# Kernel optimization log

Hardware: AMD Instinct MI355X
Metric: run time of the kernel (lower is better)

Reference implementation:

```python
import jax, jax.numpy as jnp
import numpy as np

B = 16384
D = 64            # embed_dim
N_LAYER = 2
USER_NUM, ITEM_NUM, ENTITY_NUM = 500000, 200000, 200000
H1, H2 = 128, 64  # hidden_layers
OUT_REC = 1


def setup_inputs() -> dict:
    key = jax.random.key(0)
    ks = jax.random.split(key, 24)
    f = jax.random.normal
    return {
        "user_id": jax.random.randint(ks[0], (B,), 0, USER_NUM),
        "item_id": jax.random.randint(ks[1], (B,), 0, ITEM_NUM),
        "rec_target": jax.random.uniform(ks[2], (B,), dtype=jnp.float32),
        # embedding tables
        "user_emb": f(ks[3], (USER_NUM, D), dtype=jnp.float32) * 0.01,
        "item_emb": f(ks[4], (ITEM_NUM, D), dtype=jnp.float32) * 0.01,
        "entity_emb": f(ks[5], (ENTITY_NUM, D), dtype=jnp.float32) * 0.01,
        # cross&compress parameters (torch.rand -> uniform [0,1))
        "w_vv": jax.random.uniform(ks[6], (D, 1), dtype=jnp.float32),
        "w_ev": jax.random.uniform(ks[7], (D, 1), dtype=jnp.float32),
        "w_ve": jax.random.uniform(ks[8], (D, 1), dtype=jnp.float32),
        "w_ee": jax.random.uniform(ks[9], (D, 1), dtype=jnp.float32),
        "b_v": jax.random.uniform(ks[10], (1,), dtype=jnp.float32),
        "b_e": jax.random.uniform(ks[11], (1,), dtype=jnp.float32),
        # user low MLP (embed_dim -> embed_dim)
        "Wul": f(ks[12], (D, D), dtype=jnp.float32) * (1.0 / np.sqrt(D)),
        "bul": jnp.zeros((D,), dtype=jnp.float32),
        # rec tower: 2D -> H1 -> H2 -> OUT_REC
        "W1": f(ks[13], (2 * D, H1), dtype=jnp.float32) * (1.0 / np.sqrt(2 * D)),
        "b1": jnp.zeros((H1,), dtype=jnp.float32),
        "W2": f(ks[14], (H1, H2), dtype=jnp.float32) * (1.0 / np.sqrt(H1)),
        "b2": jnp.zeros((H2,), dtype=jnp.float32),
        "W3": f(ks[15], (H2, OUT_REC), dtype=jnp.float32) * (1.0 / np.sqrt(H2)),
        "b3": jnp.zeros((OUT_REC,), dtype=jnp.float32),
    }


def _cross_compress(item, head, w_vv, w_ev, w_ve, w_ee, b_v, b_e):
    # c = item[:, :, None] * head[:, None, :]; c @ w == item * (head @ w)
    # c_t = head[:, :, None] * item[:, None, :]; c_t @ w == head * (item @ w)
    item_c = item * (head @ w_vv) + head * (item @ w_ev) + b_v
    head_c = item * (head @ w_ve) + head * (item @ w_ee) + b_e
    return item_c, head_c


def reference(user_id, item_id, rec_target, user_emb, item_emb, entity_emb,
              w_vv, w_ev, w_ve, w_ee, b_v, b_e, Wul, bul,
              W1, b1, W2, b2, W3, b3):
    # 'rec' training path (dropout disabled / eval mode)
    user = user_emb[user_id]      # [B, D]
    item = item_emb[item_id]      # [B, D]
    head = entity_emb[item_id]    # [B, D]
    for _ in range(N_LAYER):
        user = jax.nn.relu(user @ Wul + bul)
        item, head = _cross_compress(item, head, w_vv, w_ev, w_ve, w_ee, b_v, b_e)
    high = jnp.concatenate([user, item], axis=1)          # [B, 2D]
    h = jax.nn.relu(high @ W1 + b1)
    h = jax.nn.relu(h @ W2 + b2)
    rec_out = jax.nn.relu(h @ W3 + b3)                    # [B, 1]
    return rec_out.squeeze(-1), rec_target
```

## Files before the change

### kernel.cpp

```cpp
#include <hip/hip_runtime.h>


constexpr int BTOT = 16384;
constexpr int SPB  = 16;
constexpr int PAD  = 20;

__global__ __launch_bounds__(256, 4) void multikr_fused(
    const int* __restrict__ user_id, const int* __restrict__ item_id,
    const float* __restrict__ rec_target,
    const float* __restrict__ user_emb, const float* __restrict__ item_emb,
    const float* __restrict__ entity_emb,
    const float* __restrict__ w_vv, const float* __restrict__ w_ev,
    const float* __restrict__ w_ve, const float* __restrict__ w_ee,
    const float* __restrict__ b_v, const float* __restrict__ b_e,
    const float* __restrict__ Wul, const float* __restrict__ bul,
    const float* __restrict__ W1, const float* __restrict__ b1,
    const float* __restrict__ W2, const float* __restrict__ b2,
    const float* __restrict__ W3, const float* __restrict__ b3,
    float* __restrict__ out)
{
    __shared__ __align__(16) float sm[256 * PAD];
    __shared__ __align__(16) float sWul[64 * 64];
    __shared__ __align__(16) float wcT[4][64];
    __shared__ __align__(16) float scal[4][SPB];

    const int t    = threadIdx.x;
    const int lane = t & 63;
    const int wv   = t >> 6;
    const int aoff = wv << 2;
    const int s0   = blockIdx.x * SPB;

    float* U  = sm;
    float* IT = sm + 64 * PAD;
    float* HD = sm + 128 * PAD;
    float* SP = sm + 192 * PAD;

    {
        const int s = t & 15, part = t >> 4;
        const int uid = user_id[s0 + s], iid = item_id[s0 + s];
        const float4 u4 = *((const float4*)(user_emb   + (size_t)uid * 64) + part);
        const float4 i4 = *((const float4*)(item_emb   + (size_t)iid * 64) + part);
        const float4 e4 = *((const float4*)(entity_emb + (size_t)iid * 64) + part);
        const int db = part << 2;
        U [(db+0)*PAD+s]=u4.x; U [(db+1)*PAD+s]=u4.y; U [(db+2)*PAD+s]=u4.z; U [(db+3)*PAD+s]=u4.w;
        IT[(db+0)*PAD+s]=i4.x; IT[(db+1)*PAD+s]=i4.y; IT[(db+2)*PAD+s]=i4.z; IT[(db+3)*PAD+s]=i4.w;
        HD[(db+0)*PAD+s]=e4.x; HD[(db+1)*PAD+s]=e4.y; HD[(db+2)*PAD+s]=e4.z; HD[(db+3)*PAD+s]=e4.w;
        const float4* wg = (const float4*)Wul;
        float4*       ws = (float4*)sWul;
#pragma unroll
        for (int i = 0; i < 4; ++i) ws[i * 256 + t] = wg[i * 256 + t];
        if (t < 64) { wcT[0][t]=w_vv[t]; wcT[1][t]=w_ev[t]; wcT[2][t]=w_ve[t]; wcT[3][t]=w_ee[t]; }
    }
    __syncthreads();
    const float bv = b_v[0], be = b_e[0];

#pragma unroll
    for (int layer = 0; layer < 2; ++layer) {
        const float* ub = (layer == 0) ? U : SP;
        float*       vb = (layer == 0) ? SP : U;
        {
            float ua[4];
            const float bb = bul[lane];
#pragma unroll
            for (int i = 0; i < 4; ++i) ua[i] = bb;
#pragma unroll 8
            for (int d = 0; d < 64; ++d) {
                const float w = sWul[d * 64 + lane];
                const float4 av = *(const float4*)(ub + d * PAD + aoff);
                ua[0]=fmaf(av.x,w,ua[0]); ua[1]=fmaf(av.y,w,ua[1]);
                ua[2]=fmaf(av.z,w,ua[2]); ua[3]=fmaf(av.w,w,ua[3]);
            }
            *(float4*)(vb + lane * PAD + aoff) =
                make_float4(fmaxf(ua[0],0.f),fmaxf(ua[1],0.f),fmaxf(ua[2],0.f),fmaxf(ua[3],0.f));
        }
        if (lane < 16) {
            const float* src = (wv & 1) ? IT : HD;
            float a = 0.f;
#pragma unroll
            for (int dq = 0; dq < 16; ++dq) {
                const float4 w = *(const float4*)&wcT[wv][dq << 2];
                a = fmaf(src[(4*dq+0)*PAD + lane], w.x, a);
                a = fmaf(src[(4*dq+1)*PAD + lane], w.y, a);
                a = fmaf(src[(4*dq+2)*PAD + lane], w.z, a);
                a = fmaf(src[(4*dq+3)*PAD + lane], w.w, a);
            }
            scal[wv][lane] = a;
        }
        __syncthreads();
        {
            float* ip = IT + lane * PAD + aoff;
            float* hp = HD + lane * PAD + aoff;
            const float4 iv = *(const float4*)ip;
            const float4 hv = *(const float4*)hp;
            const float4 sa = *(const float4*)&scal[0][aoff];
            const float4 sb = *(const float4*)&scal[1][aoff];
            *(float4*)ip = make_float4(
                fmaf(iv.x, sa.x, fmaf(hv.x, sb.x, bv)),
                fmaf(iv.y, sa.y, fmaf(hv.y, sb.y, bv)),
                fmaf(iv.z, sa.z, fmaf(hv.z, sb.z, bv)),
                fmaf(iv.w, sa.w, fmaf(hv.w, sb.w, bv)));
            if (layer == 0) {
                const float4 sc = *(const float4*)&scal[2][aoff];
                const float4 sd = *(const float4*)&scal[3][aoff];
                *(float4*)hp = make_float4(
                    fmaf(iv.x, sc.x, fmaf(hv.x, sd.x, be)),
                    fmaf(iv.y, sc.y, fmaf(hv.y, sd.y, be)),
                    fmaf(iv.z, sc.z, fmaf(hv.z, sd.z, be)),
                    fmaf(iv.w, sc.w, fmaf(hv.w, sd.w, be)));
            }
        }
        __syncthreads();
    }

    {
        float acc0[4], acc1[4];
        const float bb0 = b1[lane], bb1 = b1[lane + 64];
#pragma unroll
        for (int i = 0; i < 4; ++i) { acc0[i] = bb0; acc1[i] = bb1; }
        float wA[16], wB[16];
        auto ldg = [&](float* buf, int dbase) {
#pragma unroll
            for (int k = 0; k < 8; ++k) {
                buf[2*k]   = W1[(dbase + k) * 128 + lane];
                buf[2*k+1] = W1[(dbase + k) * 128 + lane + 64];
            }
        };
        auto cmp = [&](const float* buf, int dbase) {
#pragma unroll
            for (int k = 0; k < 8; ++k) {
                const float4 av = *(const float4*)(sm + (dbase + k) * PAD + aoff);
                const float w0 = buf[2*k], w1 = buf[2*k+1];
                acc0[0]=fmaf(av.x,w0,acc0[0]); acc0[1]=fmaf(av.y,w0,acc0[1]);
                acc0[2]=fmaf(av.z,w0,acc0[2]); acc0[3]=fmaf(av.w,w0,acc0[3]);
                acc1[0]=fmaf(av.x,w1,acc1[0]); acc1[1]=fmaf(av.y,w1,acc1[1]);
                acc1[2]=fmaf(av.z,w1,acc1[2]); acc1[3]=fmaf(av.w,w1,acc1[3]);
            }
        };
        ldg(wA, 0);
#pragma unroll
        for (int g = 0; g < 8; ++g) {
            ldg(wB, 16*g + 8);
            cmp(wA, 16*g);
            if (g < 7) ldg(wA, 16*g + 16);
            cmp(wB, 16*g + 8);
        }
        *(float4*)(sm + (128 + lane) * PAD + aoff) =
            make_float4(fmaxf(acc0[0],0.f),fmaxf(acc0[1],0.f),fmaxf(acc0[2],0.f),fmaxf(acc0[3],0.f));
        *(float4*)(sm + (192 + lane) * PAD + aoff) =
            make_float4(fmaxf(acc1[0],0.f),fmaxf(acc1[1],0.f),fmaxf(acc1[2],0.f),fmaxf(acc1[3],0.f));
    }
    __syncthreads();

    {
        float acc[4];
        const float bb = b2[lane];
#pragma unroll
        for (int i = 0; i < 4; ++i) acc[i] = bb;
        float wA[8], wB[8];
        auto ldg = [&](float* buf, int dbase) {
#pragma unroll
            for (int k = 0; k < 8; ++k) buf[k] = W2[(dbase + k) * 64 + lane];
        };
        auto cmp = [&](const float* buf, int dbase) {
#pragma unroll
            for (int k = 0; k < 8; ++k) {
                const float4 av = *(const float4*)(sm + (128 + dbase + k) * PAD + aoff);
                const float w = buf[k];
                acc[0]=fmaf(av.x,w,acc[0]); acc[1]=fmaf(av.y,w,acc[1]);
                acc[2]=fmaf(av.z,w,acc[2]); acc[3]=fmaf(av.w,w,acc[3]);
            }
        };
        ldg(wA, 0);
#pragma unroll
        for (int g = 0; g < 8; ++g) {
            ldg(wB, 16*g + 8);
            cmp(wA, 16*g);
            if (g < 7) ldg(wA, 16*g + 16);
            cmp(wB, 16*g + 8);
        }
        *(float4*)(sm + lane * PAD + aoff) =
            make_float4(fmaxf(acc[0],0.f),fmaxf(acc[1],0.f),fmaxf(acc[2],0.f),fmaxf(acc[3],0.f));
    }
    __syncthreads();

    if (t < 64) {
        const int s = t & 15, dh = t >> 4;
        float acc = 0.f;
#pragma unroll
        for (int k = 0; k < 16; ++k) {
            const int d = 16 * dh + k;
            acc = fmaf(sm[d * PAD + s], W3[d], acc);
        }
        acc += __shfl_xor(acc, 16);
        acc += __shfl_xor(acc, 32);
        if (dh == 0) out[s0 + s] = fmaxf(acc + b3[0], 0.f);
    } else if (t < 80) {
        const int s = t - 64;
        out[BTOT + s0 + s] = rec_target[s0 + s];
    }
}

extern "C" void kernel_launch(void* const* d_in, const int* in_sizes, int n_in,
                              void* d_out, int out_size, void* d_ws, size_t ws_size,
                              hipStream_t stream) {
    (void)in_sizes; (void)n_in; (void)d_ws; (void)ws_size; (void)out_size;
    multikr_fused<<<BTOT / SPB, 256, 0, stream>>>(
        (const int*)d_in[0],  (const int*)d_in[1],  (const float*)d_in[2],
        (const float*)d_in[3], (const float*)d_in[4], (const float*)d_in[5],
        (const float*)d_in[6], (const float*)d_in[7], (const float*)d_in[8],
        (const float*)d_in[9], (const float*)d_in[10], (const float*)d_in[11],
        (const float*)d_in[12], (const float*)d_in[13], (const float*)d_in[14],
        (const float*)d_in[15], (const float*)d_in[16], (const float*)d_in[17],
        (const float*)d_in[18], (const float*)d_in[19],
        (float*)d_out);
}
```

Baseline: 258.9 us.

## Double samples per block and use register tiles in MLP layers

Raises samples per block from 16 to 32 (with a matching pad and a lower occupancy hint) and remaps the thread work so each thread computes larger register tiles: 2x4 in the user layer, 4x4 in the W1 layer and 4x2 in the W2 layer, using float4 weight loads. Cross-compress weights and W3 are kept in registers and the dot products are split over two half-waves with a shuffle reduction. The goal is to halve the per-sample global weight traffic and the number of LDS reads per FMA. In exchange the block count halves, shared memory per block roughly doubles, and register pressure rises.

Result: no change. 259.8 us (+0.3%).

```diff
diff --git a/kernel.cpp b/kernel.cpp
--- a/kernel.cpp
+++ b/kernel.cpp
@@ -2,10 +2,10 @@
 
 
 constexpr int BTOT = 16384;
-constexpr int SPB  = 16;
-constexpr int PAD  = 20;
-
-__global__ __launch_bounds__(256, 4) void multikr_fused(
+constexpr int SPB  = 32;
+constexpr int PAD  = 36;
+
+__global__ __launch_bounds__(256, 2) void multikr_fused(
     const int* __restrict__ user_id, const int* __restrict__ item_id,
     const float* __restrict__ rec_target,
     const float* __restrict__ user_emb, const float* __restrict__ item_emb,
@@ -21,13 +21,11 @@
 {
     __shared__ __align__(16) float sm[256 * PAD];
     __shared__ __align__(16) float sWul[64 * 64];
-    __shared__ __align__(16) float wcT[4][64];
     __shared__ __align__(16) float scal[4][SPB];
 
     const int t    = threadIdx.x;
     const int lane = t & 63;
     const int wv   = t >> 6;
-    const int aoff = wv << 2;
     const int s0   = blockIdx.x * SPB;
 
     float* U  = sm;
@@ -35,168 +33,210 @@
     float* HD = sm + 128 * PAD;
     float* SP = sm + 192 * PAD;
 
-    {
-        const int s = t & 15, part = t >> 4;
+    const int dh   = lane >> 5;
+    const int sdot = lane & 31;
+
+    float wcr[32];
+    {
+        const float* wsrc = (wv == 0) ? w_vv : (wv == 1) ? w_ev : (wv == 2) ? w_ve : w_ee;
+#pragma unroll
+        for (int q = 0; q < 8; ++q) {
+            const float4 w4 = *(const float4*)(wsrc + 32 * dh + 4 * q);
+            wcr[4*q] = w4.x; wcr[4*q+1] = w4.y; wcr[4*q+2] = w4.z; wcr[4*q+3] = w4.w;
+        }
+    }
+
+    {
+        const int s = t & 31, p = t >> 5;
         const int uid = user_id[s0 + s], iid = item_id[s0 + s];
-        const float4 u4 = *((const float4*)(user_emb   + (size_t)uid * 64) + part);
-        const float4 i4 = *((const float4*)(item_emb   + (size_t)iid * 64) + part);
-        const float4 e4 = *((const float4*)(entity_emb + (size_t)iid * 64) + part);
-        const int db = part << 2;
-        U [(db+0)*PAD+s]=u4.x; U [(db+1)*PAD+s]=u4.y; U [(db+2)*PAD+s]=u4.z; U [(db+3)*PAD+s]=u4.w;
-        IT[(db+0)*PAD+s]=i4.x; IT[(db+1)*PAD+s]=i4.y; IT[(db+2)*PAD+s]=i4.z; IT[(db+3)*PAD+s]=i4.w;
-        HD[(db+0)*PAD+s]=e4.x; HD[(db+1)*PAD+s]=e4.y; HD[(db+2)*PAD+s]=e4.z; HD[(db+3)*PAD+s]=e4.w;
+        const float4* ur = (const float4*)(user_emb   + (size_t)uid * 64 + 8 * p);
+        const float4* ir = (const float4*)(item_emb   + (size_t)iid * 64 + 8 * p);
+        const float4* er = (const float4*)(entity_emb + (size_t)iid * 64 + 8 * p);
+        const float4 u0 = ur[0], u1 = ur[1];
+        const float4 i0 = ir[0], i1 = ir[1];
+        const float4 e0 = er[0], e1 = er[1];
+        const int db = 8 * p;
+        U [(db+0)*PAD+s]=u0.x; U [(db+1)*PAD+s]=u0.y; U [(db+2)*PAD+s]=u0.z; U [(db+3)*PAD+s]=u0.w;
+        U [(db+4)*PAD+s]=u1.x; U [(db+5)*PAD+s]=u1.y; U [(db+6)*PAD+s]=u1.z; U [(db+7)*PAD+s]=u1.w;
+        IT[(db+0)*PAD+s]=i0.x; IT[(db+1)*PAD+s]=i0.y; IT[(db+2)*PAD+s]=i0.z; IT[(db+3)*PAD+s]=i0.w;
+        IT[(db+4)*PAD+s]=i1.x; IT[(db+5)*PAD+s]=i1.y; IT[(db+6)*PAD+s]=i1.z; IT[(db+7)*PAD+s]=i1.w;
+        HD[(db+0)*PAD+s]=e0.x; HD[(db+1)*PAD+s]=e0.y; HD[(db+2)*PAD+s]=e0.z; HD[(db+3)*PAD+s]=e0.w;
+        HD[(db+4)*PAD+s]=e1.x; HD[(db+5)*PAD+s]=e1.y; HD[(db+6)*PAD+s]=e1.z; HD[(db+7)*PAD+s]=e1.w;
         const float4* wg = (const float4*)Wul;
         float4*       ws = (float4*)sWul;
 #pragma unroll
         for (int i = 0; i < 4; ++i) ws[i * 256 + t] = wg[i * 256 + t];
-        if (t < 64) { wcT[0][t]=w_vv[t]; wcT[1][t]=w_ev[t]; wcT[2][t]=w_ve[t]; wcT[3][t]=w_ee[t]; }
     }
     __syncthreads();
     const float bv = b_v[0], be = b_e[0];
 
-#pragma unroll
-    for (int layer = 0; layer < 2; ++layer) {
-        const float* ub = (layer == 0) ? U : SP;
-        float*       vb = (layer == 0) ? SP : U;
-        {
-            float ua[4];
-            const float bb = bul[lane];
-#pragma unroll
-            for (int i = 0; i < 4; ++i) ua[i] = bb;
-#pragma unroll 8
-            for (int d = 0; d < 64; ++d) {
-                const float w = sWul[d * 64 + lane];
-                const float4 av = *(const float4*)(ub + d * PAD + aoff);
-                ua[0]=fmaf(av.x,w,ua[0]); ua[1]=fmaf(av.y,w,ua[1]);
-                ua[2]=fmaf(av.z,w,ua[2]); ua[3]=fmaf(av.w,w,ua[3]);
-            }
-            *(float4*)(vb + lane * PAD + aoff) =
-                make_float4(fmaxf(ua[0],0.f),fmaxf(ua[1],0.f),fmaxf(ua[2],0.f),fmaxf(ua[3],0.f));
-        }
-        if (lane < 16) {
-            const float* src = (wv & 1) ? IT : HD;
-            float a = 0.f;
-#pragma unroll
-            for (int dq = 0; dq < 16; ++dq) {
-                const float4 w = *(const float4*)&wcT[wv][dq << 2];
-                a = fmaf(src[(4*dq+0)*PAD + lane], w.x, a);
-                a = fmaf(src[(4*dq+1)*PAD + lane], w.y, a);
-                a = fmaf(src[(4*dq+2)*PAD + lane], w.z, a);
-                a = fmaf(src[(4*dq+3)*PAD + lane], w.w, a);
-            }
-            scal[wv][lane] = a;
-        }
-        __syncthreads();
-        {
-            float* ip = IT + lane * PAD + aoff;
-            float* hp = HD + lane * PAD + aoff;
-            const float4 iv = *(const float4*)ip;
-            const float4 hv = *(const float4*)hp;
-            const float4 sa = *(const float4*)&scal[0][aoff];
-            const float4 sb = *(const float4*)&scal[1][aoff];
-            *(float4*)ip = make_float4(
-                fmaf(iv.x, sa.x, fmaf(hv.x, sb.x, bv)),
-                fmaf(iv.y, sa.y, fmaf(hv.y, sb.y, bv)),
-                fmaf(iv.z, sa.z, fmaf(hv.z, sb.z, bv)),
-                fmaf(iv.w, sa.w, fmaf(hv.w, sb.w, bv)));
-            if (layer == 0) {
-                const float4 sc = *(const float4*)&scal[2][aoff];
-                const float4 sd = *(const float4*)&scal[3][aoff];
-                *(float4*)hp = make_float4(
-                    fmaf(iv.x, sc.x, fmaf(hv.x, sd.x, be)),
-                    fmaf(iv.y, sc.y, fmaf(hv.y, sd.y, be)),
-                    fmaf(iv.z, sc.z, fmaf(hv.z, sd.z, be)),
-                    fmaf(iv.w, sc.w, fmaf(hv.w, sd.w, be)));
-            }
-        }
-        __syncthreads();
-    }
-
-    {
-        float acc0[4], acc1[4];
-        const float bb0 = b1[lane], bb1 = b1[lane + 64];
-#pragma unroll
-        for (int i = 0; i < 4; ++i) { acc0[i] = bb0; acc1[i] = bb1; }
-        float wA[16], wB[16];
-        auto ldg = [&](float* buf, int dbase) {
+    {
+        const int cg = lane & 31;
+        const int m0 = 8 * wv + 4 * (lane >> 5);
+#pragma unroll
+        for (int layer = 0; layer < 2; ++layer) {
+            const float* ub = (layer == 0) ? U : SP;
+            float*       vb = (layer == 0) ? SP : U;
+            {
+                const float2 bb = *(const float2*)(bul + 2 * cg);
+                float a0[4] = {bb.x, bb.x, bb.x, bb.x};
+                float a1[4] = {bb.y, bb.y, bb.y, bb.y};
+#pragma unroll
+                for (int d = 0; d < 64; ++d) {
+                    const float4 av = *(const float4*)(ub + d * PAD + m0);
+                    const float2 w  = *(const float2*)(sWul + d * 64 + 2 * cg);
+                    a0[0]=fmaf(av.x,w.x,a0[0]); a0[1]=fmaf(av.y,w.x,a0[1]);
+                    a0[2]=fmaf(av.z,w.x,a0[2]); a0[3]=fmaf(av.w,w.x,a0[3]);
+                    a1[0]=fmaf(av.x,w.y,a1[0]); a1[1]=fmaf(av.y,w.y,a1[1]);
+                    a1[2]=fmaf(av.z,w.y,a1[2]); a1[3]=fmaf(av.w,w.y,a1[3]);
+                }
+                *(float4*)(vb + (2*cg    ) * PAD + m0) =
+                    make_float4(fmaxf(a0[0],0.f),fmaxf(a0[1],0.f),fmaxf(a0[2],0.f),fmaxf(a0[3],0.f));
+                *(float4*)(vb + (2*cg + 1) * PAD + m0) =
+                    make_float4(fmaxf(a1[0],0.f),fmaxf(a1[1],0.f),fmaxf(a1[2],0.f),fmaxf(a1[3],0.f));
+            }
+            {
+                const float* src = (wv & 1) ? IT : HD;
+                float a = 0.f;
+#pragma unroll
+                for (int k = 0; k < 32; ++k)
+                    a = fmaf(src[(32 * dh + k) * PAD + sdot], wcr[k], a);
+                a += __shfl_xor(a, 32);
+                if (dh == 0) scal[wv][sdot] = a;
+            }
+            __syncthreads();
+            {
+                float* ip = IT + lane * PAD + 8 * wv;
+                float* hp = HD + lane * PAD + 8 * wv;
+                const float4 iv0 = *(const float4*)(ip),     iv1 = *(const float4*)(ip + 4);
+                const float4 hv0 = *(const float4*)(hp),     hv1 = *(const float4*)(hp + 4);
+                const float4 sa0 = *(const float4*)&scal[0][8*wv], sa1 = *(const float4*)&scal[0][8*wv+4];
+                const float4 sb0 = *(const float4*)&scal[1][8*wv], sb1 = *(const float4*)&scal[1][8*wv+4];
+                *(float4*)(ip) = make_float4(
+                    fmaf(iv0.x, sa0.x, fmaf(hv0.x, sb0.x, bv)),
+                    fmaf(iv0.y, sa0.y, fmaf(hv0.y, sb0.y, bv)),
+                    fmaf(iv0.z, sa0.z, fmaf(hv0.z, sb0.z, bv)),
+                    fmaf(iv0.w, sa0.w, fmaf(hv0.w, sb0.w, bv)));
+                *(float4*)(ip + 4) = make_float4(
+                    fmaf(iv1.x, sa1.x, fmaf(hv1.x, sb1.x, bv)),
+                    fmaf(iv1.y, sa1.y, fmaf(hv1.y, sb1.y, bv)),
+                    fmaf(iv1.z, sa1.z, fmaf(hv1.z, sb1.z, bv)),
+                    fmaf(iv1.w, sa1.w, fmaf(hv1.w, sb1.w, bv)));
+                if (layer == 0) {
+                    const float4 sc0 = *(const float4*)&scal[2][8*wv], sc1 = *(const float4*)&scal[2][8*wv+4];
+                    const float4 sd0 = *(const float4*)&scal[3][8*wv], sd1 = *(const float4*)&scal[3][8*wv+4];
+                    *(float4*)(hp) = make_float4(
+                        fmaf(iv0.x, sc0.x, fmaf(hv0.x, sd0.x, be)),
+                        fmaf(iv0.y, sc0.y, fmaf(hv0.y, sd0.y, be)),
+                        fmaf(iv0.z, sc0.z, fmaf(hv0.z, sd0.z, be)),
+                        fmaf(iv0.w, sc0.w, fmaf(hv0.w, sd0.w, be)));
+                    *(float4*)(hp + 4) = make_float4(
+                        fmaf(iv1.x, sc1.x, fmaf(hv1.x, sd1.x, be)),
+                        fmaf(iv1.y, sc1.y, fmaf(hv1.y, sd1.y, be)),
+                        fmaf(iv1.z, sc1.z, fmaf(hv1.z, sd1.z, be)),
+                        fmaf(iv1.w, sc1.w, fmaf(hv1.w, sd1.w, be)));
+                }
+            }
+            __syncthreads();
+        }
+    }
+
+    {
+        const int c0  = 4 * (lane & 31);
+        const int m0h = 8 * wv + 4 * (lane >> 5);
+        float acc[4][4];
+        const float4 bb = *(const float4*)(b1 + c0);
+#pragma unroll
+        for (int i = 0; i < 4; ++i) { acc[0][i]=bb.x; acc[1][i]=bb.y; acc[2][i]=bb.z; acc[3][i]=bb.w; }
+        float4 wA[8], wB[8];
+        auto ldg = [&](float4* buf, int db) {
+#pragma unroll
+            for (int k = 0; k < 8; ++k) buf[k] = *(const float4*)(W1 + (db + k) * 128 + c0);
+        };
+        auto cmp = [&](const float4* buf, int db) {
 #pragma unroll
             for (int k = 0; k < 8; ++k) {
-                buf[2*k]   = W1[(dbase + k) * 128 + lane];
-                buf[2*k+1] = W1[(dbase + k) * 128 + lane + 64];
-            }
-        };
-        auto cmp = [&](const float* buf, int dbase) {
+                const float4 av = *(const float4*)(sm + (db + k) * PAD + m0h);
+                const float4 w  = buf[k];
+                acc[0][0]=fmaf(av.x,w.x,acc[0][0]); acc[0][1]=fmaf(av.y,w.x,acc[0][1]);
+                acc[0][2]=fmaf(av.z,w.x,acc[0][2]); acc[0][3]=fmaf(av.w,w.x,acc[0][3]);
+                acc[1][0]=fmaf(av.x,w.y,acc[1][0]); acc[1][1]=fmaf(av.y,w.y,acc[1][1]);
+                acc[1][2]=fmaf(av.z,w.y,acc[1][2]); acc[1][3]=fmaf(av.w,w.y,acc[1][3]);
+                acc[2][0]=fmaf(av.x,w.z,acc[2][0]); acc[2][1]=fmaf(av.y,w.z,acc[2][1]);
+                acc[2][2]=fmaf(av.z,w.z,acc[2][2]); acc[2][3]=fmaf(av.w,w.z,acc[2][3]);
+                acc[3][0]=fmaf(av.x,w.w,acc[3][0]); acc[3][1]=fmaf(av.y,w.w,acc[3][1]);
+                acc[3][2]=fmaf(av.z,w.w,acc[3][2]); acc[3][3]=fmaf(av.w,w.w,acc[3][3]);
+            }
+        };
+        ldg(wA, 0);
+#pragma unroll
+        for (int g = 0; g < 8; ++g) {
+            ldg(wB, 16 * g + 8);
+            cmp(wA, 16 * g);
+            if (g < 7) ldg(wA, 16 * g + 16);
+            cmp(wB, 16 * g + 8);
+        }
+#pragma unroll
+        for (int c = 0; c < 4; ++c)
+            *(float4*)(sm + (128 + c0 + c) * PAD + m0h) =
+                make_float4(fmaxf(acc[c][0],0.f),fmaxf(acc[c][1],0.f),
+                            fmaxf(acc[c][2],0.f),fmaxf(acc[c][3],0.f));
+    }
+    __syncthreads();
+
+    {
+        const int c0 = 4 * (lane & 15);
+        const int m2 = 8 * wv + 2 * (lane >> 4);
+        float acc[4][2];
+        const float4 bb = *(const float4*)(b2 + c0);
+        acc[0][0]=acc[0][1]=bb.x; acc[1][0]=acc[1][1]=bb.y;
+        acc[2][0]=acc[2][1]=bb.z; acc[3][0]=acc[3][1]=bb.w;
+        float4 wA[8], wB[8];
+        auto ldg = [&](float4* buf, int db) {
+#pragma unroll
+            for (int k = 0; k < 8; ++k) buf[k] = *(const float4*)(W2 + (db + k) * 64 + c0);
+        };
+        auto cmp = [&](const float4* buf, int db) {
 #pragma unroll
             for (int k = 0; k < 8; ++k) {
-                const float4 av = *(const float4*)(sm + (dbase + k) * PAD + aoff);
-                const float w0 = buf[2*k], w1 = buf[2*k+1];
-                acc0[0]=fmaf(av.x,w0,acc0[0]); acc0[1]=fmaf(av.y,w0,acc0[1]);
-                acc0[2]=fmaf(av.z,w0,acc0[2]); acc0[3]=fmaf(av.w,w0,acc0[3]);
-                acc1[0]=fmaf(av.x,w1,acc1[0]); acc1[1]=fmaf(av.y,w1,acc1[1]);
-                acc1[2]=fmaf(av.z,w1,acc1[2]); acc1[3]=fmaf(av.w,w1,acc1[3]);
+                const float2 av = *(const float2*)(sm + (128 + db + k) * PAD + m2);
+                const float4 w  = buf[k];
+                acc[0][0]=fmaf(av.x,w.x,acc[0][0]); acc[0][1]=fmaf(av.y,w.x,acc[0][1]);
+                acc[1][0]=fmaf(av.x,w.y,acc[1][0]); acc[1][1]=fmaf(av.y,w.y,acc[1][1]);
+                acc[2][0]=fmaf(av.x,w.z,acc[2][0]); acc[2][1]=fmaf(av.y,w.z,acc[2][1]);
+                acc[3][0]=fmaf(av.x,w.w,acc[3][0]); acc[3][1]=fmaf(av.y,w.w,acc[3][1]);
             }
         };
         ldg(wA, 0);
 #pragma unroll
         for (int g = 0; g < 8; ++g) {
-            ldg(wB, 16*g + 8);
-            cmp(wA, 16*g);
-            if (g < 7) ldg(wA, 16*g + 16);
-            cmp(wB, 16*g + 8);
-        }
-        *(float4*)(sm + (128 + lane) * PAD + aoff) =
-            make_float4(fmaxf(acc0[0],0.f),fmaxf(acc0[1],0.f),fmaxf(acc0[2],0.f),fmaxf(acc0[3],0.f));
-        *(float4*)(sm + (192 + lane) * PAD + aoff) =
-            make_float4(fmaxf(acc1[0],0.f),fmaxf(acc1[1],0.f),fmaxf(acc1[2],0.f),fmaxf(acc1[3],0.f));
+            ldg(wB, 16 * g + 8);
+            cmp(wA, 16 * g);
+            if (g < 7) ldg(wA, 16 * g + 16);
+            cmp(wB, 16 * g + 8);
+        }
+#pragma unroll
+        for (int c = 0; c < 4; ++c)
+            *(float2*)(sm + (c0 + c) * PAD + m2) =
+                make_float2(fmaxf(acc[c][0],0.f), fmaxf(acc[c][1],0.f));
     }
     __syncthreads();
 
-    {
-        float acc[4];
-        const float bb = b2[lane];
-#pragma unroll
-        for (int i = 0; i < 4; ++i) acc[i] = bb;
-        float wA[8], wB[8];
-        auto ldg = [&](float* buf, int dbase) {
-#pragma unroll
-            for (int k = 0; k < 8; ++k) buf[k] = W2[(dbase + k) * 64 + lane];
-        };
-        auto cmp = [&](const float* buf, int dbase) {
-#pragma unroll
-            for (int k = 0; k < 8; ++k) {
-                const float4 av = *(const float4*)(sm + (128 + dbase + k) * PAD + aoff);
-                const float w = buf[k];
-                acc[0]=fmaf(av.x,w,acc[0]); acc[1]=fmaf(av.y,w,acc[1]);
-                acc[2]=fmaf(av.z,w,acc[2]); acc[3]=fmaf(av.w,w,acc[3]);
-            }
-        };
-        ldg(wA, 0);
-#pragma unroll
-        for (int g = 0; g < 8; ++g) {
-            ldg(wB, 16*g + 8);
-            cmp(wA, 16*g);
-            if (g < 7) ldg(wA, 16*g + 16);
-            cmp(wB, 16*g + 8);
-        }
-        *(float4*)(sm + lane * PAD + aoff) =
-            make_float4(fmaxf(acc[0],0.f),fmaxf(acc[1],0.f),fmaxf(acc[2],0.f),fmaxf(acc[3],0.f));
-    }
-    __syncthreads();
-
-    if (t < 64) {
-        const int s = t & 15, dh = t >> 4;
-        float acc = 0.f;
-#pragma unroll
-        for (int k = 0; k < 16; ++k) {
-            const int d = 16 * dh + k;
-            acc = fmaf(sm[d * PAD + s], W3[d], acc);
-        }
-        acc += __shfl_xor(acc, 16);
-        acc += __shfl_xor(acc, 32);
-        if (dh == 0) out[s0 + s] = fmaxf(acc + b3[0], 0.f);
-    } else if (t < 80) {
-        const int s = t - 64;
-        out[BTOT + s0 + s] = rec_target[s0 + s];
+    if (wv == 0) {
+        float w3r[32];
+#pragma unroll
+        for (int q = 0; q < 8; ++q) {
+            const float4 w4 = *(const float4*)(W3 + 32 * dh + 4 * q);
+            w3r[4*q] = w4.x; w3r[4*q+1] = w4.y; w3r[4*q+2] = w4.z; w3r[4*q+3] = w4.w;
+        }
+        float a = 0.f;
+#pragma unroll
+        for (int k = 0; k < 32; ++k)
+            a = fmaf(sm[(32 * dh + k) * PAD + sdot], w3r[k], a);
+        a += __shfl_xor(a, 32);
+        if (dh == 0) out[s0 + sdot] = fmaxf(a + b3[0], 0.f);
+    } else if (wv == 1) {
+        if (lane < 32) out[BTOT + s0 + lane] = rec_target[s0 + lane];
     }
 }
 
```

## Drop shared Wul staging and remap MLP thread tiles to read weights from global

Applied to the files above, without the earlier changes.

Removes the shared-memory copy of Wul and has each thread read Wul, W1 and W2 directly from global/L1 with a new output-column/sample mapping: 16 columns by 4-sample groups per wave for the 64-wide layers, and 32 columns by 8 samples for the W1 layer. The explicit double-buffered register prefetch of W1/W2 is replaced by plain unrolled loops. The cross-compress dot products now use all lanes with shuffle reductions instead of 16 lanes per wave. The aim is to cut LDS footprint (raising occupancy) and setup traffic, at the cost of more global/L1 weight loads per block and less explicit latency hiding.

New measurement: 317.3 us. +22.5%, slower.

```diff
diff --git a/kernel.cpp b/kernel.cpp
--- a/kernel.cpp
+++ b/kernel.cpp
@@ -20,14 +20,12 @@
     float* __restrict__ out)
 {
     __shared__ __align__(16) float sm[256 * PAD];
-    __shared__ __align__(16) float sWul[64 * 64];
     __shared__ __align__(16) float wcT[4][64];
-    __shared__ __align__(16) float scal[4][SPB];
+    __shared__ float scal[4][SPB];
 
     const int t    = threadIdx.x;
     const int lane = t & 63;
     const int wv   = t >> 6;
-    const int aoff = wv << 2;
     const int s0   = blockIdx.x * SPB;
 
     float* U  = sm;
@@ -36,20 +34,17 @@
     float* SP = sm + 192 * PAD;
 
     {
-        const int s = t & 15, part = t >> 4;
+        const int s = t & 15, p = t >> 4;
         const int uid = user_id[s0 + s], iid = item_id[s0 + s];
-        const float4 u4 = *((const float4*)(user_emb   + (size_t)uid * 64) + part);
-        const float4 i4 = *((const float4*)(item_emb   + (size_t)iid * 64) + part);
-        const float4 e4 = *((const float4*)(entity_emb + (size_t)iid * 64) + part);
-        const int db = part << 2;
+        const float4 u4 = *((const float4*)(user_emb   + (size_t)uid * 64) + p);
+        const float4 i4 = *((const float4*)(item_emb   + (size_t)iid * 64) + p);
+        const float4 e4 = *((const float4*)(entity_emb + (size_t)iid * 64) + p);
+        const int db = p << 2;
         U [(db+0)*PAD+s]=u4.x; U [(db+1)*PAD+s]=u4.y; U [(db+2)*PAD+s]=u4.z; U [(db+3)*PAD+s]=u4.w;
         IT[(db+0)*PAD+s]=i4.x; IT[(db+1)*PAD+s]=i4.y; IT[(db+2)*PAD+s]=i4.z; IT[(db+3)*PAD+s]=i4.w;
         HD[(db+0)*PAD+s]=e4.x; HD[(db+1)*PAD+s]=e4.y; HD[(db+2)*PAD+s]=e4.z; HD[(db+3)*PAD+s]=e4.w;
-        const float4* wg = (const float4*)Wul;
-        float4*       ws = (float4*)sWul;
-#pragma unroll
-        for (int i = 0; i < 4; ++i) ws[i * 256 + t] = wg[i * 256 + t];
-        if (t < 64) { wcT[0][t]=w_vv[t]; wcT[1][t]=w_ev[t]; wcT[2][t]=w_ve[t]; wcT[3][t]=w_ee[t]; }
+        const float* wsrc = (wv == 0) ? w_vv : (wv == 1) ? w_ev : (wv == 2) ? w_ve : w_ee;
+        wcT[wv][lane] = wsrc[lane];
     }
     __syncthreads();
     const float bv = b_v[0], be = b_e[0];
@@ -59,49 +54,50 @@
         const float* ub = (layer == 0) ? U : SP;
         float*       vb = (layer == 0) ? SP : U;
         {
-            float ua[4];
-            const float bb = bul[lane];
+            const int cu = 16 * wv + (lane & 15);
+            const int m  = 4 * (lane >> 4);
+            float a[4];
+            const float bb = bul[cu];
 #pragma unroll
-            for (int i = 0; i < 4; ++i) ua[i] = bb;
-#pragma unroll 8
+            for (int i = 0; i < 4; ++i) a[i] = bb;
+#pragma unroll 16
             for (int d = 0; d < 64; ++d) {
-                const float w = sWul[d * 64 + lane];
-                const float4 av = *(const float4*)(ub + d * PAD + aoff);
-                ua[0]=fmaf(av.x,w,ua[0]); ua[1]=fmaf(av.y,w,ua[1]);
-                ua[2]=fmaf(av.z,w,ua[2]); ua[3]=fmaf(av.w,w,ua[3]);
+                const float  w  = Wul[d * 64 + cu];
+                const float4 av = *(const float4*)(ub + d * PAD + m);
+                a[0]=fmaf(av.x,w,a[0]); a[1]=fmaf(av.y,w,a[1]);
+                a[2]=fmaf(av.z,w,a[2]); a[3]=fmaf(av.w,w,a[3]);
             }
-            *(float4*)(vb + lane * PAD + aoff) =
-                make_float4(fmaxf(ua[0],0.f),fmaxf(ua[1],0.f),fmaxf(ua[2],0.f),fmaxf(ua[3],0.f));
+            *(float4*)(vb + cu * PAD + m) =
+                make_float4(fmaxf(a[0],0.f),fmaxf(a[1],0.f),fmaxf(a[2],0.f),fmaxf(a[3],0.f));
         }
-        if (lane < 16) {
+        {
             const float* src = (wv & 1) ? IT : HD;
+            const int s  = lane & 15;
+            const int dq = lane >> 4;
             float a = 0.f;
 #pragma unroll
-            for (int dq = 0; dq < 16; ++dq) {
-                const float4 w = *(const float4*)&wcT[wv][dq << 2];
-                a = fmaf(src[(4*dq+0)*PAD + lane], w.x, a);
-                a = fmaf(src[(4*dq+1)*PAD + lane], w.y, a);
-                a = fmaf(src[(4*dq+2)*PAD + lane], w.z, a);
-                a = fmaf(src[(4*dq+3)*PAD + lane], w.w, a);
-            }
-            scal[wv][lane] = a;
+            for (int k = 0; k < 16; ++k)
+                a = fmaf(src[(16 * dq + k) * PAD + s], wcT[wv][16 * dq + k], a);
+            a += __shfl_xor(a, 16);
+            a += __shfl_xor(a, 32);
+            if (lane < 16) scal[wv][lane] = a;
         }
         __syncthreads();
         {
-            float* ip = IT + lane * PAD + aoff;
-            float* hp = HD + lane * PAD + aoff;
+            float* ip = IT + (t & 63) * PAD + 4 * wv;
+            float* hp = HD + (t & 63) * PAD + 4 * wv;
             const float4 iv = *(const float4*)ip;
             const float4 hv = *(const float4*)hp;
-            const float4 sa = *(const float4*)&scal[0][aoff];
-            const float4 sb = *(const float4*)&scal[1][aoff];
+            const float4 sa = *(const float4*)&scal[0][4 * wv];
+            const float4 sb = *(const float4*)&scal[1][4 * wv];
             *(float4*)ip = make_float4(
                 fmaf(iv.x, sa.x, fmaf(hv.x, sb.x, bv)),
                 fmaf(iv.y, sa.y, fmaf(hv.y, sb.y, bv)),
                 fmaf(iv.z, sa.z, fmaf(hv.z, sb.z, bv)),
                 fmaf(iv.w, sa.w, fmaf(hv.w, sb.w, bv)));
             if (layer == 0) {
-                const float4 sc = *(const float4*)&scal[2][aoff];
-                const float4 sd = *(const float4*)&scal[3][aoff];
+                const float4 sc = *(const float4*)&scal[2][4 * wv];
+                const float4 sd = *(const float4*)&scal[3][4 * wv];
                 *(float4*)hp = make_float4(
                     fmaf(iv.x, sc.x, fmaf(hv.x, sd.x, be)),
                     fmaf(iv.y, sc.y, fmaf(hv.y, sd.y, be)),
@@ -113,90 +109,66 @@
     }
 
     {
-        float acc0[4], acc1[4];
-        const float bb0 = b1[lane], bb1 = b1[lane + 64];
+        const int c = 32 * wv + (lane & 31);
+        const int m = 8 * (lane >> 5);
+        float acc[8];
+        const float bb = b1[c];
 #pragma unroll
-        for (int i = 0; i < 4; ++i) { acc0[i] = bb0; acc1[i] = bb1; }
-        float wA[16], wB[16];
-        auto ldg = [&](float* buf, int dbase) {
-#pragma unroll
-            for (int k = 0; k < 8; ++k) {
-                buf[2*k]   = W1[(dbase + k) * 128 + lane];
-                buf[2*k+1] = W1[(dbase + k) * 128 + lane + 64];
-            }
-        };
-        auto cmp = [&](const float* buf, int dbase) {
-#pragma unroll
-            for (int k = 0; k < 8; ++k) {
-                const float4 av = *(const float4*)(sm + (dbase + k) * PAD + aoff);
-                const float w0 = buf[2*k], w1 = buf[2*k+1];
-                acc0[0]=fmaf(av.x,w0,acc0[0]); acc0[1]=fmaf(av.y,w0,acc0[1]);
-                acc0[2]=fmaf(av.z,w0,acc0[2]); acc0[3]=fmaf(av.w,w0,acc0[3]);
-                acc1[0]=fmaf(av.x,w1,acc1[0]); acc1[1]=fmaf(av.y,w1,acc1[1]);
-                acc1[2]=fmaf(av.z,w1,acc1[2]); acc1[3]=fmaf(av.w,w1,acc1[3]);
-            }
-        };
-        ldg(wA, 0);
-#pragma unroll
-        for (int g = 0; g < 8; ++g) {
-            ldg(wB, 16*g + 8);
-            cmp(wA, 16*g);
-            if (g < 7) ldg(wA, 16*g + 16);
-            cmp(wB, 16*g + 8);
+        for (int i = 0; i < 8; ++i) acc[i] = bb;
+#pragma unroll 16
+        for (int d = 0; d < 128; ++d) {
+            const float  w   = W1[d * 128 + c];
+            const float4 av0 = *(const float4*)(sm + d * PAD + m);
+            const float4 av1 = *(const float4*)(sm + d * PAD + m + 4);
+            acc[0]=fmaf(av0.x,w,acc[0]); acc[1]=fmaf(av0.y,w,acc[1]);
+            acc[2]=fmaf(av0.z,w,acc[2]); acc[3]=fmaf(av0.w,w,acc[3]);
+            acc[4]=fmaf(av1.x,w,acc[4]); acc[5]=fmaf(av1.y,w,acc[5]);
+            acc[6]=fmaf(av1.z,w,acc[6]); acc[7]=fmaf(av1.w,w,acc[7]);
         }
-        *(float4*)(sm + (128 + lane) * PAD + aoff) =
-            make_float4(fmaxf(acc0[0],0.f),fmaxf(acc0[1],0.f),fmaxf(acc0[2],0.f),fmaxf(acc0[3],0.f));
-        *(float4*)(sm + (192 + lane) * PAD + aoff) =
-            make_float4(fmaxf(acc1[0],0.f),fmaxf(acc1[1],0.f),fmaxf(acc1[2],0.f),fmaxf(acc1[3],0.f));
+        float* dst = sm + (128 + c) * PAD + m;
+        *(float4*)(dst)     = make_float4(fmaxf(acc[0],0.f),fmaxf(acc[1],0.f),
+                                          fmaxf(acc[2],0.f),fmaxf(acc[3],0.f));
+        *(float4*)(dst + 4) = make_float4(fmaxf(acc[4],0.f),fmaxf(acc[5],0.f),
+                                          fmaxf(acc[6],0.f),fmaxf(acc[7],0.f));
     }
     __syncthreads();
 
     {
+        const int c = 16 * wv + (lane & 15);
+        const int m = 4 * (lane >> 4);
         float acc[4];
-        const float bb = b2[lane];
+        const float bb = b2[c];
 #pragma unroll
         for (int i = 0; i < 4; ++i) acc[i] = bb;
-        float wA[8], wB[8];
-        auto ldg = [&](float* buf, int dbase) {
-#pragma unroll
-            for (int k = 0; k < 8; ++k) buf[k] = W2[(dbase + k) * 64 + lane];
-        };
-        auto cmp = [&](const float* buf, int dbase) {
-#pragma unroll
-            for (int k = 0; k < 8; ++k) {
-                const float4 av = *(const float4*)(sm + (128 + dbase + k) * PAD + aoff);
-                const float w = buf[k];
-                acc[0]=fmaf(av.x,w,acc[0]); acc[1]=fmaf(av.y,w,acc[1]);
-                acc[2]=fmaf(av.z,w,acc[2]); acc[3]=fmaf(av.w,w,acc[3]);
-            }
-        };
-        ldg(wA, 0);
-#pragma unroll
-        for (int g = 0; g < 8; ++g) {
-            ldg(wB, 16*g + 8);
-            cmp(wA, 16*g);
-            if (g < 7) ldg(wA, 16*g + 16);
-            cmp(wB, 16*g + 8);
+#pragma unroll 16
+        for (int d = 0; d < 128; ++d) {
+            const float  w  = W2[d * 64 + c];
+            const float4 av = *(const float4*)(sm + (128 + d) * PAD + m);
+            acc[0]=fmaf(av.x,w,acc[0]); acc[1]=fmaf(av.y,w,acc[1]);
+            acc[2]=fmaf(av.z,w,acc[2]); acc[3]=fmaf(av.w,w,acc[3]);
         }
-        *(float4*)(sm + lane * PAD + aoff) =
+        *(float4*)(sm + c * PAD + m) =
             make_float4(fmaxf(acc[0],0.f),fmaxf(acc[1],0.f),fmaxf(acc[2],0.f),fmaxf(acc[3],0.f));
     }
     __syncthreads();
 
-    if (t < 64) {
-        const int s = t & 15, dh = t >> 4;
-        float acc = 0.f;
+    if (wv == 0) {
+        const int s = lane & 15, dq = lane >> 4;
+        float w3r[16];
 #pragma unroll
-        for (int k = 0; k < 16; ++k) {
-            const int d = 16 * dh + k;
-            acc = fmaf(sm[d * PAD + s], W3[d], acc);
+        for (int q = 0; q < 4; ++q) {
+            const float4 w4 = *(const float4*)(W3 + 16 * dq + 4 * q);
+            w3r[4*q]=w4.x; w3r[4*q+1]=w4.y; w3r[4*q+2]=w4.z; w3r[4*q+3]=w4.w;
         }
-        acc += __shfl_xor(acc, 16);
-        acc += __shfl_xor(acc, 32);
-        if (dh == 0) out[s0 + s] = fmaxf(acc + b3[0], 0.f);
-    } else if (t < 80) {
-        const int s = t - 64;
-        out[BTOT + s0 + s] = rec_target[s0 + s];
+        float a = 0.f;
+#pragma unroll
+        for (int k = 0; k < 16; ++k)
+            a = fmaf(sm[(16 * dq + k) * PAD + s], w3r[k], a);
+        a += __shfl_xor(a, 16);
+        a += __shfl_xor(a, 32);
+        if (lane < 16) out[s0 + s] = fmaxf(a + b3[0], 0.f);
+    } else if (wv == 1) {
+        if (lane < 16) out[BTOT + s0 + lane] = rec_target[s0 + lane];
     }
 }
 
```
